# Optimization experiments

Hardware: AMD Instinct MI355X
Metric: run time of the kernel (lower is better)

Reference implementation:

```python
import jax, jax.numpy as jnp
import numpy as np

N = 100000
E = 640000
IN_CH = 256
OUT_CH = 64
HID = 2 * OUT_CH  # 128


def setup_inputs() -> dict:
    key = jax.random.key(0)
    ks = jax.random.split(key, 8)
    x = jax.random.normal(ks[0], (N, IN_CH), dtype=jnp.float32)
    edge_index = jax.random.randint(ks[1], (2, E), 0, N, dtype=jnp.int32)
    s = 1.0 / np.sqrt(IN_CH)
    W1 = jax.random.uniform(ks[2], (IN_CH, HID), jnp.float32, -s, s)
    b1 = jnp.zeros((HID,), jnp.float32)
    s2 = 1.0 / np.sqrt(HID)
    W_mu = jax.random.uniform(ks[3], (HID, OUT_CH), jnp.float32, -s2, s2)
    b_mu = jnp.zeros((OUT_CH,), jnp.float32)
    W_ls = jax.random.uniform(ks[4], (HID, OUT_CH), jnp.float32, -s2, s2)
    b_ls = jnp.zeros((OUT_CH,), jnp.float32)
    return {"x": x, "W1": W1, "b1": b1, "W_mu": W_mu, "b_mu": b_mu,
            "W_ls": W_ls, "b_ls": b_ls, "edge_index": edge_index}


def _gcn_norm(edge_index, n_nodes):
    # PyG GCNConv default: add self-loops, symmetric normalization D^-1/2 A D^-1/2
    loops = jnp.arange(n_nodes, dtype=edge_index.dtype)
    src = jnp.concatenate([edge_index[0], loops])
    dst = jnp.concatenate([edge_index[1], loops])
    deg = jax.ops.segment_sum(jnp.ones_like(dst, jnp.float32), dst, num_segments=n_nodes)
    dinv = jnp.where(deg > 0, jax.lax.rsqrt(deg), 0.0)
    norm = dinv[src] * dinv[dst]  # [E+N]
    return src, dst, norm


def _gcn_conv(x, W, b, src, dst, norm, n_nodes):
    h = x @ W                                   # [N, F_out]
    msg = h[src] * norm[:, None]                # [E+N, F_out] gather
    out = jax.ops.segment_sum(msg, dst, num_segments=n_nodes)  # scatter-add
    return out + b


def reference(x, W1, b1, W_mu, b_mu, W_ls, b_ls, edge_index):
    src, dst, norm = _gcn_norm(edge_index, N)
    h = jax.nn.relu(_gcn_conv(x, W1, b1, src, dst, norm, N))
    mu = _gcn_conv(h, W_mu, b_mu, src, dst, norm, N)
    logstd = _gcn_conv(h, W_ls, b_ls, src, dst, norm, N)
    return mu, logstd
```

## Files before the change

kernel.cpp:

```cpp
#include <hip/hip_runtime.h>
#include <math.h>

#define NN 100000
#define EE 640000
#define INCH 256
#define HIDC 128
#define OUTC 64
#define NCHUNK ((NN + 255) / 256)

typedef __attribute__((ext_vector_type(8))) short short8;
typedef __attribute__((ext_vector_type(8))) unsigned short ushort8;
typedef __attribute__((ext_vector_type(4))) float floatx4;

__device__ __forceinline__ short f2bf(float f) {
    unsigned u = __float_as_uint(f);
    u += 0x7fff + ((u >> 16) & 1);
    return (short)(u >> 16);
}

__device__ __forceinline__ float bf2f(unsigned short u) {
    return __uint_as_float(((unsigned)u) << 16);
}

__device__ __forceinline__ unsigned pk2bf(float lo, float hi) {
    unsigned r;
    asm("v_cvt_pk_bf16_f32 %0, %1, %2" : "=v"(r) : "v"(lo), "v"(hi));
    return r;
}

__device__ __forceinline__ void async_copy16(const void* g, void* l) {
    __builtin_amdgcn_global_load_lds(
        (const __attribute__((address_space(1))) unsigned int*)g,
        (__attribute__((address_space(3))) unsigned int*)l,
        16, 0, 0);
}

__global__ void k_deg_zero(int* __restrict__ deg) {
    int i = blockIdx.x * 256 + threadIdx.x;
    if (i < NN) deg[i] = 0;
}

__global__ void k_deg_count(const int* __restrict__ dstp, int* __restrict__ deg) {
    int e = blockIdx.x * 256 + threadIdx.x;
    if (e < EE) atomicAdd(&deg[dstp[e]], 1);
}

__global__ __launch_bounds__(256) void k_scan1(const int* __restrict__ deg,
                                               int* __restrict__ partials) {
    int i = blockIdx.x * 256 + threadIdx.x;
    int v = (i < NN) ? deg[i] : 0;
    for (int o = 32; o; o >>= 1) v += __shfl_down(v, o, 64);
    __shared__ int sm[4];
    if ((threadIdx.x & 63) == 0) sm[threadIdx.x >> 6] = v;
    __syncthreads();
    if (threadIdx.x == 0) partials[blockIdx.x] = sm[0] + sm[1] + sm[2] + sm[3];
}

__global__ __launch_bounds__(512) void k_scan2(int* __restrict__ partials) {
    __shared__ int sm[512];
    int t = threadIdx.x;
    int v = (t < NCHUNK) ? partials[t] : 0;
    sm[t] = v;
    __syncthreads();
    for (int o = 1; o < 512; o <<= 1) {
        int add = (t >= o) ? sm[t - o] : 0;
        __syncthreads();
        sm[t] += add;
        __syncthreads();
    }
    if (t < NCHUNK) partials[t] = sm[t] - v;
}

__global__ __launch_bounds__(256) void k_scan3(const int* __restrict__ deg,
                                               const int* __restrict__ partials,
                                               int* __restrict__ row_off,
                                               int* __restrict__ cursor,
                                               float* __restrict__ dinv) {
    int t = threadIdx.x;
    int i = blockIdx.x * 256 + t;
    int v = (i < NN) ? deg[i] : 0;
    __shared__ int sm[256];
    sm[t] = v;
    __syncthreads();
    for (int o = 1; o < 256; o <<= 1) {
        int add = (t >= o) ? sm[t - o] : 0;
        __syncthreads();
        sm[t] += add;
        __syncthreads();
    }
    if (i < NN) {
        int excl = partials[blockIdx.x] + sm[t] - v;
        row_off[i] = excl;
        cursor[i] = excl;
        dinv[i] = rsqrtf((float)(v + 1));
    }
}

__global__ void k_fill(const int* __restrict__ srcp, const int* __restrict__ dstp,
                       int* __restrict__ cursor, int* __restrict__ esrc) {
    int e = blockIdx.x * 256 + threadIdx.x;
    if (e < EE) {
        int d = dstp[e];
        int pos = atomicAdd(&cursor[d], 1);
        esrc[pos] = srcp[e];
    }
}

__global__ void k_prep(const float* __restrict__ W1,
                       const float* __restrict__ Wmu, const float* __restrict__ bmu,
                       const float* __restrict__ Wls, const float* __restrict__ bls,
                       short* __restrict__ wt, short* __restrict__ wct,
                       float* __restrict__ bcat) {
    int i = blockIdx.x * 256 + threadIdx.x;
    if (i < 32768) {
        int n = i >> 8, k = i & 255;
        wt[i] = f2bf(W1[k * HIDC + n]);
    } else if (i < 32768 + 16384) {
        int j = i - 32768;
        int n = j >> 7, k = j & 127;
        float v = (n < OUTC) ? Wmu[k * OUTC + n] : Wls[k * OUTC + (n - OUTC)];
        wct[j] = f2bf(v);
    } else if (i < 32768 + 16384 + 128) {
        int c = i - (32768 + 16384);
        bcat[c] = (c < OUTC) ? bmu[c] : bls[c - OUTC];
    }
}

__global__ __launch_bounds__(256, 2) void k_mgemm1(const float* __restrict__ x,
                                                   const short* __restrict__ wt,
                                                   short* __restrict__ out) {
    __shared__ __align__(16) float xs[2][64 * 128];
    int wave = threadIdx.x >> 6;
    int lane = threadIdx.x & 63;
    int m = lane & 15, quad = lane >> 4;
    int rbase = blockIdx.x * 64;

#pragma unroll
    for (int i = 0; i < 8; i++) {
        int r = wave * 16 + 2 * i + (lane >> 5);
        int grow = rbase + r; if (grow >= NN) grow = NN - 1;
        int chunk = (lane & 31) ^ (r & 7);
        const float* gsrc = x + (size_t)grow * INCH + chunk * 4;
        float* ldst = xs[0] + (wave * 16 + 2 * i) * 128;
        async_copy16(gsrc, ldst);
    }

    short8 bfr[2][8];
#pragma unroll
    for (int ct = 0; ct < 2; ct++)
#pragma unroll
        for (int kg = 0; kg < 8; kg++)
            bfr[ct][kg] = *(const short8*)(wt + (size_t)(wave * 32 + ct * 16 + m) * INCH
                                              + kg * 32 + quad * 8);

#pragma unroll
    for (int i = 0; i < 8; i++) {
        int r = wave * 16 + 2 * i + (lane >> 5);
        int grow = rbase + r; if (grow >= NN) grow = NN - 1;
        int chunk = (lane & 31) ^ (r & 7);
        const float* gsrc = x + (size_t)grow * INCH + 128 + chunk * 4;
        float* ldst = xs[1] + (wave * 16 + 2 * i) * 128;
        async_copy16(gsrc, ldst);
    }

    floatx4 acc[4][2];
#pragma unroll
    for (int rt = 0; rt < 4; rt++) { acc[rt][0] = (floatx4)(0.f); acc[rt][1] = (floatx4)(0.f); }

#define COMPUTE_HALF(h)                                                                  \
    _Pragma("unroll")                                                                    \
    for (int k0 = 0; k0 < 4; k0++) {                                                     \
        int cb = k0 * 8 + (quad << 1);                       \
        _Pragma("unroll")                                                                \
        for (int rt = 0; rt < 4; rt++) {                                                 \
            int r = rt * 16 + m;                                                         \
            int key = m & 7;                                     \
            const float* p0 = xs[h] + r * 128 + (((cb) ^ key) << 2);                     \
            const float* p1 = xs[h] + r * 128 + (((cb + 1) ^ key) << 2);                 \
            float4 f0 = *(const float4*)p0;                                              \
            float4 f1 = *(const float4*)p1;                                              \
            union { short8 s; unsigned u[4]; } a;                                        \
            a.u[0] = pk2bf(f0.x, f0.y); a.u[1] = pk2bf(f0.z, f0.w);                      \
            a.u[2] = pk2bf(f1.x, f1.y); a.u[3] = pk2bf(f1.z, f1.w);                      \
            acc[rt][0] = __builtin_amdgcn_mfma_f32_16x16x32_bf16(a.s, bfr[0][(h)*4+k0],  \
                                                                 acc[rt][0], 0, 0, 0);   \
            acc[rt][1] = __builtin_amdgcn_mfma_f32_16x16x32_bf16(a.s, bfr[1][(h)*4+k0],  \
                                                                 acc[rt][1], 0, 0, 0);   \
        }                                                                                \
    }

    asm volatile("s_waitcnt vmcnt(8)" ::: "memory");
    __builtin_amdgcn_sched_barrier(0);
    __builtin_amdgcn_s_barrier();
    COMPUTE_HALF(0)
    asm volatile("s_waitcnt vmcnt(0)" ::: "memory");
    __builtin_amdgcn_sched_barrier(0);
    __builtin_amdgcn_s_barrier();
    COMPUTE_HALF(1)
#undef COMPUTE_HALF

#pragma unroll
    for (int rt = 0; rt < 4; rt++) {
        int rs = rbase + rt * 16 + quad * 4;
#pragma unroll
        for (int ct = 0; ct < 2; ct++) {
            int c = wave * 32 + ct * 16 + m;
#pragma unroll
            for (int r = 0; r < 4; r++) {
                int rr = rs + r;
                if (rr < NN) out[(size_t)rr * HIDC + c] = f2bf(acc[rt][ct][r]);
            }
        }
    }
}

__global__ __launch_bounds__(256, 1) void k_mgemm2(const short* __restrict__ agg,
                                                   const short* __restrict__ wct,
                                                   const float* __restrict__ bcat,
                                                   float* __restrict__ out) {
    int wave = threadIdx.x >> 6;
    int lane = threadIdx.x & 63;
    int rhalf = wave & 1, chalf = wave >> 1;
    int m = lane & 15, quad = lane >> 4;
    int rbase = blockIdx.x * 64 + rhalf * 32;
    int r0c = min(rbase + m, NN - 1);
    int r1c = min(rbase + 16 + m, NN - 1);
    const short* ar0 = agg + (size_t)r0c * HIDC + quad * 8;
    const short* ar1 = agg + (size_t)r1c * HIDC + quad * 8;

    short8 pa0[4], pa1[4];
#pragma unroll
    for (int c = 0; c < 4; c++) {
        pa0[c] = *(const short8*)(ar0 + c * 32);
        pa1[c] = *(const short8*)(ar1 + c * 32);
    }
    __builtin_amdgcn_sched_barrier(0);

    const short* wbase = wct + quad * 8 + (size_t)m * HIDC + (size_t)(chalf * 4) * 16 * HIDC;
    floatx4 acc0[4], acc1[4];
#pragma unroll
    for (int i = 0; i < 4; i++) { acc0[i] = (floatx4)(0.f); acc1[i] = (floatx4)(0.f); }
#pragma unroll
    for (int k = 0; k < 4; k++) {
        const short* wq = wbase + k * 32;
#pragma unroll
        for (int nt = 0; nt < 4; nt++) {
            short8 b = *(const short8*)(wq + (size_t)nt * 16 * HIDC);
            acc0[nt] = __builtin_amdgcn_mfma_f32_16x16x32_bf16(pa0[k], b, acc0[nt], 0, 0, 0);
            acc1[nt] = __builtin_amdgcn_mfma_f32_16x16x32_bf16(pa1[k], b, acc1[nt], 0, 0, 0);
        }
    }
    int rs0 = rbase + quad * 4;
    int rs1 = rbase + 16 + quad * 4;
#pragma unroll
    for (int nt = 0; nt < 4; nt++) {
        int c = (chalf * 4 + nt) * 16 + m;
        float bv = bcat[c];
        float* obase = (c < OUTC) ? (out + c) : (out + (size_t)NN * OUTC + (c - OUTC));
#pragma unroll
        for (int r = 0; r < 4; r++) {
            int rr = rs0 + r;
            if (rr < NN) obase[(size_t)rr * OUTC] = acc0[nt][r] + bv;
            int rr2 = rs1 + r;
            if (rr2 < NN) obase[(size_t)rr2 * OUTC] = acc1[nt][r] + bv;
        }
    }
}

template <bool RELU>
__global__ __launch_bounds__(256) void k_gather(const short* __restrict__ feat,
                                                const int* __restrict__ esrc,
                                                const int* __restrict__ row_off,
                                                const int* __restrict__ deg,
                                                const float* __restrict__ dinv,
                                                const float* __restrict__ bias,
                                                short* __restrict__ out) {
    int gid = blockIdx.x * 256 + threadIdx.x;
    int d = gid >> 4;
    int l = threadIdx.x & 15;
    if (d >= NN) return;
    const ushort8* fp = (const ushort8*)feat;
    float dd = dinv[d];
    float sw = dd * dd;
    ushort8 sv = fp[(size_t)d * 16 + l];
    float acc[8];
#pragma unroll
    for (int i = 0; i < 8; i++) acc[i] = bf2f(sv[i]) * sw;
    int off = row_off[d];
    int cnt = deg[d];
    for (int base = 0; base < cnt; base += 16) {
        int mm = min(16, cnt - base);
        int sj = (l < mm) ? esrc[off + base + l] : 0;
        float dj = (l < mm) ? dinv[sj] : 0.f;
        int j = 0;
        for (; j + 4 <= mm; j += 4) {
            int s0 = __shfl(sj, j + 0, 16);
            int s1 = __shfl(sj, j + 1, 16);
            int s2 = __shfl(sj, j + 2, 16);
            int s3 = __shfl(sj, j + 3, 16);
            float n0 = __shfl(dj, j + 0, 16) * dd;
            float n1 = __shfl(dj, j + 1, 16) * dd;
            float n2 = __shfl(dj, j + 2, 16) * dd;
            float n3 = __shfl(dj, j + 3, 16) * dd;
            ushort8 v0 = fp[(size_t)s0 * 16 + l];
            ushort8 v1 = fp[(size_t)s1 * 16 + l];
            ushort8 v2 = fp[(size_t)s2 * 16 + l];
            ushort8 v3 = fp[(size_t)s3 * 16 + l];
#pragma unroll
            for (int i = 0; i < 8; i++) acc[i] = fmaf(bf2f(v0[i]), n0, acc[i]);
#pragma unroll
            for (int i = 0; i < 8; i++) acc[i] = fmaf(bf2f(v1[i]), n1, acc[i]);
#pragma unroll
            for (int i = 0; i < 8; i++) acc[i] = fmaf(bf2f(v2[i]), n2, acc[i]);
#pragma unroll
            for (int i = 0; i < 8; i++) acc[i] = fmaf(bf2f(v3[i]), n3, acc[i]);
        }
        if (j + 2 <= mm) {
            int s0 = __shfl(sj, j + 0, 16);
            int s1 = __shfl(sj, j + 1, 16);
            float n0 = __shfl(dj, j + 0, 16) * dd;
            float n1 = __shfl(dj, j + 1, 16) * dd;
            ushort8 v0 = fp[(size_t)s0 * 16 + l];
            ushort8 v1 = fp[(size_t)s1 * 16 + l];
#pragma unroll
            for (int i = 0; i < 8; i++) acc[i] = fmaf(bf2f(v0[i]), n0, acc[i]);
#pragma unroll
            for (int i = 0; i < 8; i++) acc[i] = fmaf(bf2f(v1[i]), n1, acc[i]);
            j += 2;
        }
        if (j < mm) {
            int s0 = __shfl(sj, j, 16);
            float n0 = __shfl(dj, j, 16) * dd;
            ushort8 v0 = fp[(size_t)s0 * 16 + l];
#pragma unroll
            for (int i = 0; i < 8; i++) acc[i] = fmaf(bf2f(v0[i]), n0, acc[i]);
        }
    }
    if (RELU) {
        float4 b0 = *(const float4*)(bias + l * 8);
        float4 b1 = *(const float4*)(bias + l * 8 + 4);
        acc[0] = fmaxf(acc[0] + b0.x, 0.f);
        acc[1] = fmaxf(acc[1] + b0.y, 0.f);
        acc[2] = fmaxf(acc[2] + b0.z, 0.f);
        acc[3] = fmaxf(acc[3] + b0.w, 0.f);
        acc[4] = fmaxf(acc[4] + b1.x, 0.f);
        acc[5] = fmaxf(acc[5] + b1.y, 0.f);
        acc[6] = fmaxf(acc[6] + b1.z, 0.f);
        acc[7] = fmaxf(acc[7] + b1.w, 0.f);
    }
    ushort8 o;
#pragma unroll
    for (int i = 0; i < 8; i++) o[i] = (unsigned short)f2bf(acc[i]);
    ((ushort8*)out)[(size_t)d * 16 + l] = o;
}

extern "C" void kernel_launch(void* const* d_in, const int* in_sizes, int n_in,
                              void* d_out, int out_size, void* d_ws, size_t ws_size,
                              hipStream_t stream) {
    const float* x   = (const float*)d_in[0];
    const float* W1  = (const float*)d_in[1];
    const float* b1  = (const float*)d_in[2];
    const float* Wmu = (const float*)d_in[3];
    const float* bmu = (const float*)d_in[4];
    const float* Wls = (const float*)d_in[5];
    const float* bls = (const float*)d_in[6];
    const int*   ei  = (const int*)d_in[7];
    const int* srcp = ei;
    const int* dstp = ei + EE;

    float* out = (float*)d_out;

    char* wsb = (char*)d_ws;
    short* bufA    = (short*)wsb;
    short* bufH    = bufA + (size_t)NN * HIDC;
    int*   deg     = (int*)(bufH + (size_t)NN * HIDC);
    int*   row_off = deg + NN;
    int*   cursor  = row_off + NN;
    float* dinv    = (float*)(cursor + NN);
    int*   esrc    = (int*)(dinv + NN);
    int*   partials = esrc + EE;
    short* wt      = (short*)(partials + NCHUNK + 1);
    short* wct     = wt + 128 * 256;
    float* bcat    = (float*)(wct + 128 * 128);

    const int nb_n = (NN + 255) / 256;
    const int nb_e = (EE + 255) / 256;
    const int nb_g = (NN * 16) / 256;
    const int nb_m = (NN + 63) / 64;

    k_deg_zero<<<nb_n, 256, 0, stream>>>(deg);
    k_deg_count<<<nb_e, 256, 0, stream>>>(dstp, deg);
    k_scan1<<<NCHUNK, 256, 0, stream>>>(deg, partials);
    k_scan2<<<1, 512, 0, stream>>>(partials);
    k_scan3<<<NCHUNK, 256, 0, stream>>>(deg, partials, row_off, cursor, dinv);
    k_fill<<<nb_e, 256, 0, stream>>>(srcp, dstp, cursor, esrc);
    k_prep<<<193, 256, 0, stream>>>(W1, Wmu, bmu, Wls, bls, wt, wct, bcat);

    k_mgemm1<<<nb_m, 256, 0, stream>>>(x, wt, bufA);
    k_gather<true><<<nb_g, 256, 0, stream>>>(bufA, esrc, row_off, deg, dinv, b1, bufH);

    k_gather<false><<<nb_g, 256, 0, stream>>>(bufH, esrc, row_off, deg, dinv, nullptr, bufA);
    k_mgemm2<<<nb_m, 256, 0, stream>>>(bufA, wct, bcat, out);
}
```

Measured before the change: 347.7 us.

## Fuse prep/scan kernels, use memset, and halve GEMM1 row tile

Removes the separate zeroing, scan2 and weight-prep kernels. Zeroing becomes a hipMemsetAsync, weight prep is folded into scan1, and each scan3 block now sums the earlier block partials itself. The first GEMM's row tile drops from 64 to 32 with occupancy hint 4, halving shared memory per block and dropping the bounds checks since N divides by 32. This cuts launch overhead and serial scan steps, at the cost of redundant partial sums in scan3 and less weight-fragment reuse per block in GEMM1.

Measured after the change: 348.6 us. No clear change (+0.2%).

```diff
diff --git a/kernel.cpp b/kernel.cpp
--- a/kernel.cpp
+++ b/kernel.cpp
@@ -35,19 +35,34 @@
         16, 0, 0);
 }
 
-__global__ void k_deg_zero(int* __restrict__ deg) {
-    int i = blockIdx.x * 256 + threadIdx.x;
-    if (i < NN) deg[i] = 0;
-}
-
 __global__ void k_deg_count(const int* __restrict__ dstp, int* __restrict__ deg) {
     int e = blockIdx.x * 256 + threadIdx.x;
     if (e < EE) atomicAdd(&deg[dstp[e]], 1);
 }
 
 __global__ __launch_bounds__(256) void k_scan1(const int* __restrict__ deg,
-                                               int* __restrict__ partials) {
+                                               int* __restrict__ partials,
+                                               const float* __restrict__ W1,
+                                               const float* __restrict__ Wmu,
+                                               const float* __restrict__ bmu,
+                                               const float* __restrict__ Wls,
+                                               const float* __restrict__ bls,
+                                               short* __restrict__ wt,
+                                               short* __restrict__ wct,
+                                               float* __restrict__ bcat) {
     int i = blockIdx.x * 256 + threadIdx.x;
+    if (i < 32768) {
+        int n = i >> 8, k = i & 255;
+        wt[i] = f2bf(W1[k * HIDC + n]);
+    } else if (i < 49152) {
+        int j = i - 32768;
+        int n = j >> 7, k = j & 127;
+        float v = (n < OUTC) ? Wmu[k * OUTC + n] : Wls[k * OUTC + (n - OUTC)];
+        wct[j] = f2bf(v);
+    } else if (i < 49280) {
+        int c = i - 49152;
+        bcat[c] = (c < OUTC) ? bmu[c] : bls[c - OUTC];
+    }
     int v = (i < NN) ? deg[i] : 0;
     for (int o = 32; o; o >>= 1) v += __shfl_down(v, o, 64);
     __shared__ int sm[4];
@@ -56,27 +71,19 @@
     if (threadIdx.x == 0) partials[blockIdx.x] = sm[0] + sm[1] + sm[2] + sm[3];
 }
 
-__global__ __launch_bounds__(512) void k_scan2(int* __restrict__ partials) {
-    __shared__ int sm[512];
-    int t = threadIdx.x;
-    int v = (t < NCHUNK) ? partials[t] : 0;
-    sm[t] = v;
-    __syncthreads();
-    for (int o = 1; o < 512; o <<= 1) {
-        int add = (t >= o) ? sm[t - o] : 0;
-        __syncthreads();
-        sm[t] += add;
-        __syncthreads();
-    }
-    if (t < NCHUNK) partials[t] = sm[t] - v;
-}
-
 __global__ __launch_bounds__(256) void k_scan3(const int* __restrict__ deg,
                                                const int* __restrict__ partials,
                                                int* __restrict__ row_off,
                                                int* __restrict__ cursor,
                                                float* __restrict__ dinv) {
     int t = threadIdx.x;
+    int pacc = 0;
+    for (int b = t; b < blockIdx.x; b += 256) pacc += partials[b];
+    for (int o = 32; o; o >>= 1) pacc += __shfl_down(pacc, o, 64);
+    __shared__ int pg[4];
+    if ((t & 63) == 0) pg[t >> 6] = pacc;
+    __syncthreads();
+    int blockoff = pg[0] + pg[1] + pg[2] + pg[3];
     int i = blockIdx.x * 256 + t;
     int v = (i < NN) ? deg[i] : 0;
     __shared__ int sm[256];
@@ -89,7 +96,7 @@
         __syncthreads();
     }
     if (i < NN) {
-        int excl = partials[blockIdx.x] + sm[t] - v;
+        int excl = blockoff + sm[t] - v;
         row_off[i] = excl;
         cursor[i] = excl;
         dinv[i] = rsqrtf((float)(v + 1));
@@ -106,42 +113,21 @@
     }
 }
 
-__global__ void k_prep(const float* __restrict__ W1,
-                       const float* __restrict__ Wmu, const float* __restrict__ bmu,
-                       const float* __restrict__ Wls, const float* __restrict__ bls,
-                       short* __restrict__ wt, short* __restrict__ wct,
-                       float* __restrict__ bcat) {
-    int i = blockIdx.x * 256 + threadIdx.x;
-    if (i < 32768) {
-        int n = i >> 8, k = i & 255;
-        wt[i] = f2bf(W1[k * HIDC + n]);
-    } else if (i < 32768 + 16384) {
-        int j = i - 32768;
-        int n = j >> 7, k = j & 127;
-        float v = (n < OUTC) ? Wmu[k * OUTC + n] : Wls[k * OUTC + (n - OUTC)];
-        wct[j] = f2bf(v);
-    } else if (i < 32768 + 16384 + 128) {
-        int c = i - (32768 + 16384);
-        bcat[c] = (c < OUTC) ? bmu[c] : bls[c - OUTC];
-    }
-}
-
-__global__ __launch_bounds__(256, 2) void k_mgemm1(const float* __restrict__ x,
+__global__ __launch_bounds__(256, 4) void k_mgemm1(const float* __restrict__ x,
                                                    const short* __restrict__ wt,
                                                    short* __restrict__ out) {
-    __shared__ __align__(16) float xs[2][64 * 128];
+    __shared__ __align__(16) float xs[2][32 * 128];
     int wave = threadIdx.x >> 6;
     int lane = threadIdx.x & 63;
     int m = lane & 15, quad = lane >> 4;
-    int rbase = blockIdx.x * 64;
-
-#pragma unroll
-    for (int i = 0; i < 8; i++) {
-        int r = wave * 16 + 2 * i + (lane >> 5);
-        int grow = rbase + r; if (grow >= NN) grow = NN - 1;
+    int rbase = blockIdx.x * 32;
+
+#pragma unroll
+    for (int i = 0; i < 4; i++) {
+        int r = wave * 8 + 2 * i + (lane >> 5);
         int chunk = (lane & 31) ^ (r & 7);
-        const float* gsrc = x + (size_t)grow * INCH + chunk * 4;
-        float* ldst = xs[0] + (wave * 16 + 2 * i) * 128;
+        const float* gsrc = x + (size_t)(rbase + r) * INCH + chunk * 4;
+        float* ldst = xs[0] + (wave * 8 + 2 * i) * 128;
         async_copy16(gsrc, ldst);
     }
 
@@ -154,27 +140,26 @@
                                               + kg * 32 + quad * 8);
 
 #pragma unroll
-    for (int i = 0; i < 8; i++) {
-        int r = wave * 16 + 2 * i + (lane >> 5);
-        int grow = rbase + r; if (grow >= NN) grow = NN - 1;
+    for (int i = 0; i < 4; i++) {
+        int r = wave * 8 + 2 * i + (lane >> 5);
         int chunk = (lane & 31) ^ (r & 7);
-        const float* gsrc = x + (size_t)grow * INCH + 128 + chunk * 4;
-        float* ldst = xs[1] + (wave * 16 + 2 * i) * 128;
+        const float* gsrc = x + (size_t)(rbase + r) * INCH + 128 + chunk * 4;
+        float* ldst = xs[1] + (wave * 8 + 2 * i) * 128;
         async_copy16(gsrc, ldst);
     }
 
-    floatx4 acc[4][2];
-#pragma unroll
-    for (int rt = 0; rt < 4; rt++) { acc[rt][0] = (floatx4)(0.f); acc[rt][1] = (floatx4)(0.f); }
+    floatx4 acc[2][2];
+#pragma unroll
+    for (int rt = 0; rt < 2; rt++) { acc[rt][0] = (floatx4)(0.f); acc[rt][1] = (floatx4)(0.f); }
 
 #define COMPUTE_HALF(h)                                                                  \
     _Pragma("unroll")                                                                    \
     for (int k0 = 0; k0 < 4; k0++) {                                                     \
         int cb = k0 * 8 + (quad << 1);                       \
         _Pragma("unroll")                                                                \
-        for (int rt = 0; rt < 4; rt++) {                                                 \
+        for (int rt = 0; rt < 2; rt++) {                                                 \
             int r = rt * 16 + m;                                                         \
-            int key = m & 7;                                     \
+            int key = m & 7;                                                             \
             const float* p0 = xs[h] + r * 128 + (((cb) ^ key) << 2);                     \
             const float* p1 = xs[h] + r * 128 + (((cb + 1) ^ key) << 2);                 \
             float4 f0 = *(const float4*)p0;                                              \
@@ -189,7 +174,7 @@
         }                                                                                \
     }
 
-    asm volatile("s_waitcnt vmcnt(8)" ::: "memory");
+    asm volatile("s_waitcnt vmcnt(4)" ::: "memory");
     __builtin_amdgcn_sched_barrier(0);
     __builtin_amdgcn_s_barrier();
     COMPUTE_HALF(0)
@@ -200,15 +185,14 @@
 #undef COMPUTE_HALF
 
 #pragma unroll
-    for (int rt = 0; rt < 4; rt++) {
+    for (int rt = 0; rt < 2; rt++) {
         int rs = rbase + rt * 16 + quad * 4;
 #pragma unroll
         for (int ct = 0; ct < 2; ct++) {
             int c = wave * 32 + ct * 16 + m;
 #pragma unroll
             for (int r = 0; r < 4; r++) {
-                int rr = rs + r;
-                if (rr < NN) out[(size_t)rr * HIDC + c] = f2bf(acc[rt][ct][r]);
+                out[(size_t)(rs + r) * HIDC + c] = f2bf(acc[rt][ct][r]);
             }
         }
     }
@@ -383,22 +367,20 @@
     short* wct     = wt + 128 * 256;
     float* bcat    = (float*)(wct + 128 * 128);
 
-    const int nb_n = (NN + 255) / 256;
     const int nb_e = (EE + 255) / 256;
     const int nb_g = (NN * 16) / 256;
-    const int nb_m = (NN + 63) / 64;
-
-    k_deg_zero<<<nb_n, 256, 0, stream>>>(deg);
+    const int nb_m1 = NN / 32;
+    const int nb_m2 = (NN + 63) / 64;
+
+    hipMemsetAsync(deg, 0, NN * sizeof(int), stream);
     k_deg_count<<<nb_e, 256, 0, stream>>>(dstp, deg);
-    k_scan1<<<NCHUNK, 256, 0, stream>>>(deg, partials);
-    k_scan2<<<1, 512, 0, stream>>>(partials);
+    k_scan1<<<NCHUNK, 256, 0, stream>>>(deg, partials, W1, Wmu, bmu, Wls, bls, wt, wct, bcat);
     k_scan3<<<NCHUNK, 256, 0, stream>>>(deg, partials, row_off, cursor, dinv);
     k_fill<<<nb_e, 256, 0, stream>>>(srcp, dstp, cursor, esrc);
-    k_prep<<<193, 256, 0, stream>>>(W1, Wmu, bmu, Wls, bls, wt, wct, bcat);
-
-    k_mgemm1<<<nb_m, 256, 0, stream>>>(x, wt, bufA);
+
+    k_mgemm1<<<nb_m1, 256, 0, stream>>>(x, wt, bufA);
     k_gather<true><<<nb_g, 256, 0, stream>>>(bufA, esrc, row_off, deg, dinv, b1, bufH);
 
     k_gather<false><<<nb_g, 256, 0, stream>>>(bufH, esrc, row_off, deg, dinv, nullptr, bufA);
-    k_mgemm2<<<nb_m, 256, 0, stream>>>(bufA, wct, bcat, out);
-}
+    k_mgemm2<<<nb_m2, 256, 0, stream>>>(bufA, wct, bcat, out);
+}
```
